# Performance work log

Hardware: AMD Instinct MI355X
Metric: run time of the kernel (lower is better)

## Reference

```python
import jax, jax.numpy as jnp
import numpy as np

NEG_BIG = -9e15
ALPHA = 0.2  # leaky relu slope


def setup_inputs() -> dict:
    key = jax.random.key(0)
    k1, k2, k3, k4 = jax.random.split(key, 4)
    B, N, Fin, Fout = 8, 2048, 128, 64
    h = jax.random.normal(k1, (B, N, Fin), dtype=jnp.float32)
    adj = jax.random.randint(k2, (B, N, N), 0, 2, dtype=jnp.int32)
    # xavier_uniform-like init scale
    W = jax.random.uniform(k3, (Fin, Fout), dtype=jnp.float32, minval=-1.0, maxval=1.0) * (1.414 * np.sqrt(6.0 / (Fin + Fout)))
    a = jax.random.uniform(k4, (2 * Fout, 1), dtype=jnp.float32, minval=-1.0, maxval=1.0) * (1.414 * np.sqrt(6.0 / (2 * Fout + 1)))
    return {"h": h, "adj": adj, "W": W, "a": a}


def reference(h, adj, W, a):
    # h: [B,N,Fin], adj: [B,N,N], W: [Fin,Fout], a: [2*Fout,1]
    Fout = W.shape[1]
    Wh = jnp.einsum('bni,io->bno', h, W)            # [B,N,Fout]
    # e_ij = leakyrelu(a[:Fout] . Wh_i + a[Fout:] . Wh_j)  (decomposed, same math
    # as the original concat + matmul with a)
    f_src = Wh @ a[:Fout, 0]                        # [B,N]
    f_dst = Wh @ a[Fout:, 0]                        # [B,N]
    e = f_src[:, :, None] + f_dst[:, None, :]       # [B,N,N]
    e = jnp.where(e > 0, e, ALPHA * e)              # leaky relu
    e = jnp.where(adj > 0, e, NEG_BIG)              # mask
    attention = jax.nn.softmax(e, axis=2)           # [B,N,N]
    h_prime = jnp.einsum('bnm,bmo->bno', attention, Wh)
    return jax.nn.elu(h_prime)
```

## Files before the change

kernel.cpp:

```cpp
#include <hip/hip_runtime.h>
#include <hip/hip_bf16.h>

constexpr int Bb  = 8;
constexpr int Nn  = 2048;
constexpr int FIN = 128;
constexpr int FOUT = 64;
constexpr float LOG2E = 1.4426950408889634f;

typedef __bf16 bf16x8 __attribute__((ext_vector_type(8)));
typedef __bf16 bf16x2 __attribute__((ext_vector_type(2)));
typedef float  f32x4  __attribute__((ext_vector_type(4)));
typedef int    i32x4  __attribute__((ext_vector_type(4)));
typedef unsigned int u32;

__device__ __forceinline__ u32 f2bf_bits(float f) {
    u32 u = __builtin_bit_cast(u32, f);
    return (u + 0x7FFFu + ((u >> 16) & 1u)) >> 16;
}

__global__ __launch_bounds__(256) void gat_k1(
        const float* __restrict__ h, const float* __restrict__ W,
        const float* __restrict__ a, __bf16* __restrict__ whfrag,
        float* __restrict__ fs, float* __restrict__ fd) {
    const int blk = blockIdx.x;
    const int b   = blk >> 6;
    const int t32 = blk & 63;
    const int n0  = t32 * 32;
    const int l   = threadIdx.x & 63;
    const int w   = __builtin_amdgcn_readfirstlane((int)(threadIdx.x >> 6));

    __shared__ __align__(16) float hT[32][FIN];

    {
        const float4* hb = reinterpret_cast<const float4*>(h + (size_t)(b * Nn + n0) * FIN);
        float4* dst = reinterpret_cast<float4*>(&hT[0][0]);
#pragma unroll
        for (int k = 0; k < 4; ++k) {
            const int flat = threadIdx.x + k * 256;
            dst[flat] = hb[flat];
        }
    }
    __syncthreads();

    const float a0 = a[l];
    const float a1 = a[FOUT + l];

    float acc[8];
#pragma unroll
    for (int r = 0; r < 8; ++r) acc[r] = 0.f;

#pragma unroll 1
    for (int c0 = 0; c0 < FIN; c0 += 32) {
        float wreg[32];
#pragma unroll
        for (int cc = 0; cc < 32; ++cc) wreg[cc] = W[(c0 + cc) * FOUT + l];
#pragma unroll
        for (int r = 0; r < 8; ++r) {
            const int row = w * 8 + r;
#pragma unroll
            for (int cc = 0; cc < 32; ++cc)
                acc[r] = fmaf(hT[row][c0 + cc], wreg[cc], acc[r]);
        }
    }

#pragma unroll
    for (int r = 0; r < 8; ++r) {
        float s0 = acc[r] * a0;
        float s1 = acc[r] * a1;
#pragma unroll
        for (int off = 32; off >= 1; off >>= 1) {
            s0 += __shfl_xor(s0, off, 64);
            s1 += __shfl_xor(s1, off, 64);
        }
        if (l == 0) {
            fs[b * Nn + n0 + w * 8 + r] = s0 * LOG2E;
            fd[b * Nn + n0 + w * 8 + r] = s1 * LOG2E;
        }
    }

    u32 pk[4];
#pragma unroll
    for (int i = 0; i < 4; ++i)
        pk[i] = f2bf_bits(acc[2 * i]) | (f2bf_bits(acc[2 * i + 1]) << 16);
    const int slotg = ((b * 64 + t32) * 4 + (l >> 4)) * 64 + ((w << 4) | (l & 15));
    reinterpret_cast<uint4*>(whfrag)[slotg] = make_uint4(pk[0], pk[1], pk[2], pk[3]);
}

__global__ __launch_bounds__(256, 4) void gat_k2(
        const int* __restrict__ adj, const __bf16* __restrict__ whfrag,
        const float* __restrict__ fs, const float* __restrict__ fd,
        float* __restrict__ out) {
    const int blk = blockIdx.x;
    const int b   = blk >> 7;
    const int i0  = (blk & 127) * 16;
    const int l   = threadIdx.x & 63;
    const int w   = __builtin_amdgcn_readfirstlane((int)(threadIdx.x >> 6));

    __shared__ __align__(16) char  aLDS[4 * 4096];
    __shared__ f32x4 comb[4][4][64];
    __shared__ float zpart[4][16];

    const int g  = l >> 4;
    const int jc = l & 15;

    char* myA = aLDS + w * 4096;

    float fs_loc[4];
#pragma unroll
    for (int rr = 0; rr < 4; ++rr) fs_loc[rr] = fs[b * Nn + i0 + g * 4 + rr];

    const int    jq0  = w * 512;
    const float* fdp  = fd + b * Nn + jq0 + jc * 4;
    const int*   adj0 = adj + (size_t)(b * Nn + i0 + g * 4) * Nn + jq0 + jc * 4;

    const bf16x8* bfr = reinterpret_cast<const bf16x8*>(whfrag)
                        + (size_t)((b * 64 + w * 16) * 4) * 64 + l;

    f32x4 acc[4] = {{0,0,0,0},{0,0,0,0},{0,0,0,0},{0,0,0,0}};
    f32x4 accz   = {0.f, 0.f, 0.f, 0.f};

    bf16x8 onesv;
#pragma unroll
    for (int i = 0; i < 8; ++i) onesv[i] = (__bf16)1.0f;

    i32x4 adjR[3][4];
    f32x4 fdR[3];

#pragma unroll
    for (int rr = 0; rr < 4; ++rr) {
        adjR[0][rr] = *reinterpret_cast<const i32x4*>(adj0 + (size_t)rr * Nn);
        adjR[1][rr] = *reinterpret_cast<const i32x4*>(adj0 + (size_t)rr * Nn + 64);
    }
    fdR[0] = *reinterpret_cast<const f32x4*>(fdp);
    fdR[1] = *reinterpret_cast<const f32x4*>(fdp + 64);

#define GAT_STEP(IT, CUR, PRE)                                                 \
  {                                                                            \
    if ((IT) + 2 < 8) {                \
      _Pragma("unroll")                                                        \
      for (int rr = 0; rr < 4; ++rr)                                           \
        adjR[PRE][rr] = *reinterpret_cast<const i32x4*>(                       \
            adj0 + (size_t)rr * Nn + ((IT) + 2) * 64);                         \
      fdR[PRE] = *reinterpret_cast<const f32x4*>(fdp + ((IT) + 2) * 64);       \
    }                                                                          \
    char* buf = myA + ((IT) & 1) * 2048;                                       \
    _Pragma("unroll")                                                          \
    for (int rr = 0; rr < 4; ++rr) {                                           \
      const int row = g * 4 + rr;                                              \
      u32 wds[2];                                                              \
      _Pragma("unroll")                                                        \
      for (int hp = 0; hp < 2; ++hp) {                                         \
        float pv[2];                                                           \
        _Pragma("unroll")                                                      \
        for (int q = 0; q < 2; ++q) {                                          \
          const int jj = hp * 2 + q;                                           \
          float e  = fs_loc[rr] + fdR[CUR][jj];                                \
          float lr = fmaxf(e, 0.2f * e);          \
          float p  = exp2f(lr);                 \
          pv[q] = (adjR[CUR][rr][jj] > 0) ? p : 0.f;                           \
        }                                                                      \
        wds[hp] = __builtin_bit_cast(u32,                                      \
                      (bf16x2){(__bf16)pv[0], (__bf16)pv[1]});                 \
      }                                                                        \
      const int boff = (row * 128 + jc * 8) ^ ((row & 7) << 4);                \
      *reinterpret_cast<uint2*>(buf + boff) = make_uint2(wds[0], wds[1]);      \
    }                                                                          \
    asm volatile("s_waitcnt lgkmcnt(0)" ::: "memory");                         \
    __builtin_amdgcn_sched_barrier(0x20);            \
    {                                                                          \
      const int rb0 = (((l & 15) * 128 + g * 16) ^ ((l & 7) << 4));            \
      bf16x8 av = *reinterpret_cast<const bf16x8*>(buf + rb0);                 \
      _Pragma("unroll")                                                        \
      for (int o16 = 0; o16 < 4; ++o16)                                        \
        acc[o16] = __builtin_amdgcn_mfma_f32_16x16x32_bf16(                    \
            av, bfr[(((IT) * 2 + 0) * 4 + o16) * 64], acc[o16], 0, 0, 0);      \
      accz = __builtin_amdgcn_mfma_f32_16x16x32_bf16(av, onesv, accz, 0, 0, 0);\
    }                                                                          \
    {                                                                          \
      const int rb1 = (((l & 15) * 128 + 64 + g * 16) ^ ((l & 7) << 4));       \
      bf16x8 av = *reinterpret_cast<const bf16x8*>(buf + rb1);                 \
      _Pragma("unroll")                                                        \
      for (int o16 = 0; o16 < 4; ++o16)                                        \
        acc[o16] = __builtin_amdgcn_mfma_f32_16x16x32_bf16(                    \
            av, bfr[(((IT) * 2 + 1) * 4 + o16) * 64], acc[o16], 0, 0, 0);      \
      accz = __builtin_amdgcn_mfma_f32_16x16x32_bf16(av, onesv, accz, 0, 0, 0);\
    }                                                                          \
  }

    GAT_STEP(0, 0, 2)
    GAT_STEP(1, 1, 0)
    GAT_STEP(2, 2, 1)
    GAT_STEP(3, 0, 2)
    GAT_STEP(4, 1, 0)
    GAT_STEP(5, 2, 1)
    GAT_STEP(6, 0, 2)
    GAT_STEP(7, 1, 0)
#undef GAT_STEP

    if ((l & 15) == 0) {
#pragma unroll
        for (int r = 0; r < 4; ++r) zpart[w][(l >> 4) * 4 + r] = accz[r];
    }
#pragma unroll
    for (int o16 = 0; o16 < 4; ++o16) comb[w][o16][l] = acc[o16];
    __syncthreads();

    f32x4 res = comb[0][w][l];
#pragma unroll
    for (int wp = 1; wp < 4; ++wp) res += comb[wp][w][l];

#pragma unroll
    for (int r = 0; r < 4; ++r) {
        const int row = g * 4 + r;
        float z = zpart[0][row] + zpart[1][row] + zpart[2][row] + zpart[3][row];
        float v = res[r] / z;
        v = v > 0.f ? v : expm1f(v);
        out[(size_t)(b * Nn + i0 + row) * FOUT + w * 16 + jc] = v;
    }
}

extern "C" void kernel_launch(void* const* d_in, const int* in_sizes, int n_in,
                              void* d_out, int out_size, void* d_ws, size_t ws_size,
                              hipStream_t stream) {
    const float* h   = (const float*)d_in[0];
    const int*   adj = (const int*)d_in[1];
    const float* W   = (const float*)d_in[2];
    const float* a   = (const float*)d_in[3];
    float* out = (float*)d_out;

    __bf16* whfrag = (__bf16*)d_ws;
    float*  fs     = (float*)((char*)d_ws + (size_t)Bb * Nn * FOUT * 2);
    float*  fd     = fs + Bb * Nn;

    gat_k1<<<dim3(Bb * 64), dim3(256), 0, stream>>>(h, W, a, whfrag, fs, fd);
    gat_k2<<<dim3(Bb * 128), dim3(256), 0, stream>>>(adj, whfrag, fs, fd, out);
}
```

Baseline: 47.58 us.

## Pre-pack adjacency into bitmasks in a fused pre-kernel and consume bits in the attention kernel

```diff
diff --git a/kernel.cpp b/kernel.cpp
--- a/kernel.cpp
+++ b/kernel.cpp
@@ -10,26 +10,48 @@
 typedef __bf16 bf16x8 __attribute__((ext_vector_type(8)));
 typedef __bf16 bf16x2 __attribute__((ext_vector_type(2)));
 typedef float  f32x4  __attribute__((ext_vector_type(4)));
-typedef int    i32x4  __attribute__((ext_vector_type(4)));
 typedef unsigned int u32;
+typedef unsigned long long u64;
 
 __device__ __forceinline__ u32 f2bf_bits(float f) {
     u32 u = __builtin_bit_cast(u32, f);
     return (u + 0x7FFFu + ((u >> 16) & 1u)) >> 16;
 }
 
-__global__ __launch_bounds__(256) void gat_k1(
-        const float* __restrict__ h, const float* __restrict__ W,
-        const float* __restrict__ a, __bf16* __restrict__ whfrag,
-        float* __restrict__ fs, float* __restrict__ fd) {
+__global__ __launch_bounds__(256) void gat_k01(
+        const float* __restrict__ h, const int* __restrict__ adj,
+        const float* __restrict__ W, const float* __restrict__ a,
+        __bf16* __restrict__ whfrag, float* __restrict__ fs,
+        float* __restrict__ fd, u64* __restrict__ mask) {
+    __shared__ __align__(16) float hT[32][FIN];
+
+    const int l = threadIdx.x & 63;
+    const int w = __builtin_amdgcn_readfirstlane((int)(threadIdx.x >> 6));
+
+    if (blockIdx.x >= 512) {
+        const size_t gw = (size_t)(blockIdx.x - 512) * 4 + w;
+        const int* p   = adj + gw * 4096 + l;
+        u64* mout      = mask + gw * 64;
+#pragma unroll 1
+        for (int i = 0; i < 64; i += 8) {
+            int v[8];
+#pragma unroll
+            for (int k = 0; k < 8; ++k) v[k] = p[(i + k) * 64];
+            u64 m[8];
+#pragma unroll
+            for (int k = 0; k < 8; ++k) m[k] = __ballot(v[k] > 0);
+            if (l == 0) {
+#pragma unroll
+                for (int k = 0; k < 8; ++k) mout[i + k] = m[k];
+            }
+        }
+        return;
+    }
+
     const int blk = blockIdx.x;
     const int b   = blk >> 6;
     const int t32 = blk & 63;
     const int n0  = t32 * 32;
-    const int l   = threadIdx.x & 63;
-    const int w   = __builtin_amdgcn_readfirstlane((int)(threadIdx.x >> 6));
-
-    __shared__ __align__(16) float hT[32][FIN];
 
     {
         const float4* hb = reinterpret_cast<const float4*>(h + (size_t)(b * Nn + n0) * FIN);
@@ -87,7 +109,7 @@
 }
 
 __global__ __launch_bounds__(256, 4) void gat_k2(
-        const int* __restrict__ adj, const __bf16* __restrict__ whfrag,
+        const u64* __restrict__ mask, const __bf16* __restrict__ whfrag,
         const float* __restrict__ fs, const float* __restrict__ fd,
         float* __restrict__ out) {
     const int blk = blockIdx.x;
@@ -102,6 +124,7 @@
 
     const int g  = l >> 4;
     const int jc = l & 15;
+    const int shl = jc * 4;
 
     char* myA = aLDS + w * 4096;
 
@@ -111,7 +134,7 @@
 
     const int    jq0  = w * 512;
     const float* fdp  = fd + b * Nn + jq0 + jc * 4;
-    const int*   adj0 = adj + (size_t)(b * Nn + i0 + g * 4) * Nn + jq0 + jc * 4;
+    const u64*   mkp  = mask + (size_t)(b * Nn + i0 + g * 4) * 32 + w * 8;
 
     const bf16x8* bfr = reinterpret_cast<const bf16x8*>(whfrag)
                         + (size_t)((b * 64 + w * 16) * 4) * 64 + l;
@@ -123,13 +146,13 @@
 #pragma unroll
     for (int i = 0; i < 8; ++i) onesv[i] = (__bf16)1.0f;
 
-    i32x4 adjR[3][4];
+    u64   maskR[3][4];
     f32x4 fdR[3];
 
 #pragma unroll
     for (int rr = 0; rr < 4; ++rr) {
-        adjR[0][rr] = *reinterpret_cast<const i32x4*>(adj0 + (size_t)rr * Nn);
-        adjR[1][rr] = *reinterpret_cast<const i32x4*>(adj0 + (size_t)rr * Nn + 64);
+        maskR[0][rr] = mkp[rr * 32 + 0];
+        maskR[1][rr] = mkp[rr * 32 + 1];
     }
     fdR[0] = *reinterpret_cast<const f32x4*>(fdp);
     fdR[1] = *reinterpret_cast<const f32x4*>(fdp + 64);
@@ -139,14 +162,14 @@
     if ((IT) + 2 < 8) {                \
       _Pragma("unroll")                                                        \
       for (int rr = 0; rr < 4; ++rr)                                           \
-        adjR[PRE][rr] = *reinterpret_cast<const i32x4*>(                       \
-            adj0 + (size_t)rr * Nn + ((IT) + 2) * 64);                         \
+        maskR[PRE][rr] = mkp[rr * 32 + (IT) + 2];                              \
       fdR[PRE] = *reinterpret_cast<const f32x4*>(fdp + ((IT) + 2) * 64);       \
     }                                                                          \
     char* buf = myA + ((IT) & 1) * 2048;                                       \
     _Pragma("unroll")                                                          \
     for (int rr = 0; rr < 4; ++rr) {                                           \
       const int row = g * 4 + rr;                                              \
+      const u32 mm = (u32)(maskR[CUR][rr] >> shl);  \
       u32 wds[2];                                                              \
       _Pragma("unroll")                                                        \
       for (int hp = 0; hp < 2; ++hp) {                                         \
@@ -157,7 +180,7 @@
           float e  = fs_loc[rr] + fdR[CUR][jj];                                \
           float lr = fmaxf(e, 0.2f * e);          \
           float p  = exp2f(lr);                 \
-          pv[q] = (adjR[CUR][rr][jj] > 0) ? p : 0.f;                           \
+          pv[q] = ((mm >> jj) & 1u) ? p : 0.f;                                 \
         }                                                                      \
         wds[hp] = __builtin_bit_cast(u32,                                      \
                       (bf16x2){(__bf16)pv[0], (__bf16)pv[1]});                 \
@@ -231,7 +254,8 @@
     __bf16* whfrag = (__bf16*)d_ws;
     float*  fs     = (float*)((char*)d_ws + (size_t)Bb * Nn * FOUT * 2);
     float*  fd     = fs + Bb * Nn;
-
-    gat_k1<<<dim3(Bb * 64), dim3(256), 0, stream>>>(h, W, a, whfrag, fs, fd);
-    gat_k2<<<dim3(Bb * 128), dim3(256), 0, stream>>>(adj, whfrag, fs, fd, out);
-}
+    u64*    mask   = (u64*)((char*)d_ws + (4u << 20));
+
+    gat_k01<<<dim3(512 + 2048), dim3(256), 0, stream>>>(h, adj, W, a, whfrag, fs, fd, mask);
+    gat_k2 <<<dim3(Bb * 128),   dim3(256), 0, stream>>>(mask, whfrag, fs, fd, out);
+}
```

New measurement: 52.08 us. 9.4% more time.

## Fuse projection and attention kernels via cooperative launch with grid sync

Applied to the files above, without the earlier changes.

```diff
diff --git a/kernel.cpp b/kernel.cpp
--- a/kernel.cpp
+++ b/kernel.cpp
@@ -1,5 +1,8 @@
 #include <hip/hip_runtime.h>
 #include <hip/hip_bf16.h>
+#include <hip/hip_cooperative_groups.h>
+
+namespace cg = cooperative_groups;
 
 constexpr int Bb  = 8;
 constexpr int Nn  = 2048;
@@ -18,36 +21,25 @@
     return (u + 0x7FFFu + ((u >> 16) & 1u)) >> 16;
 }
 
-__global__ __launch_bounds__(256) void gat_k1(
+__device__ __forceinline__ void k1_body(
         const float* __restrict__ h, const float* __restrict__ W,
         const float* __restrict__ a, __bf16* __restrict__ whfrag,
-        float* __restrict__ fs, float* __restrict__ fd) {
-    const int blk = blockIdx.x;
-    const int b   = blk >> 6;
-    const int t32 = blk & 63;
-    const int n0  = t32 * 32;
-    const int l   = threadIdx.x & 63;
-    const int w   = __builtin_amdgcn_readfirstlane((int)(threadIdx.x >> 6));
-
-    __shared__ __align__(16) float hT[32][FIN];
-
+        float* __restrict__ fsg, float* __restrict__ fd, float* fs_lds,
+        float (*hT)[FIN], int b, int i0, int l, int w, int tid) {
     {
-        const float4* hb = reinterpret_cast<const float4*>(h + (size_t)(b * Nn + n0) * FIN);
+        const float4* hb = reinterpret_cast<const float4*>(h + (size_t)(b * Nn + i0) * FIN);
         float4* dst = reinterpret_cast<float4*>(&hT[0][0]);
-#pragma unroll
-        for (int k = 0; k < 4; ++k) {
-            const int flat = threadIdx.x + k * 256;
-            dst[flat] = hb[flat];
-        }
+        dst[tid]       = hb[tid];
+        dst[tid + 256] = hb[tid + 256];
     }
     __syncthreads();
 
     const float a0 = a[l];
     const float a1 = a[FOUT + l];
 
-    float acc[8];
-#pragma unroll
-    for (int r = 0; r < 8; ++r) acc[r] = 0.f;
+    float acc[4];
+#pragma unroll
+    for (int r = 0; r < 4; ++r) acc[r] = 0.f;
 
 #pragma unroll 1
     for (int c0 = 0; c0 < FIN; c0 += 32) {
@@ -55,8 +47,8 @@
 #pragma unroll
         for (int cc = 0; cc < 32; ++cc) wreg[cc] = W[(c0 + cc) * FOUT + l];
 #pragma unroll
-        for (int r = 0; r < 8; ++r) {
-            const int row = w * 8 + r;
+        for (int r = 0; r < 4; ++r) {
+            const int row = w * 4 + r;
 #pragma unroll
             for (int cc = 0; cc < 32; ++cc)
                 acc[r] = fmaf(hT[row][c0 + cc], wreg[cc], acc[r]);
@@ -64,7 +56,7 @@
     }
 
 #pragma unroll
-    for (int r = 0; r < 8; ++r) {
+    for (int r = 0; r < 4; ++r) {
         float s0 = acc[r] * a0;
         float s1 = acc[r] * a1;
 #pragma unroll
@@ -73,49 +65,28 @@
             s1 += __shfl_xor(s1, off, 64);
         }
         if (l == 0) {
-            fs[b * Nn + n0 + w * 8 + r] = s0 * LOG2E;
-            fd[b * Nn + n0 + w * 8 + r] = s1 * LOG2E;
+            fs_lds[w * 4 + r] = s0 * LOG2E;
+            fsg[b * Nn + i0 + w * 4 + r] = s0 * LOG2E;
+            fd [b * Nn + i0 + w * 4 + r] = s1 * LOG2E;
         }
     }
 
-    u32 pk[4];
-#pragma unroll
-    for (int i = 0; i < 4; ++i)
-        pk[i] = f2bf_bits(acc[2 * i]) | (f2bf_bits(acc[2 * i + 1]) << 16);
-    const int slotg = ((b * 64 + t32) * 4 + (l >> 4)) * 64 + ((w << 4) | (l & 15));
-    reinterpret_cast<uint4*>(whfrag)[slotg] = make_uint4(pk[0], pk[1], pk[2], pk[3]);
-}
-
-__global__ __launch_bounds__(256, 4) void gat_k2(
-        const int* __restrict__ adj, const __bf16* __restrict__ whfrag,
-        const float* __restrict__ fs, const float* __restrict__ fd,
-        float* __restrict__ out) {
-    const int blk = blockIdx.x;
-    const int b   = blk >> 7;
-    const int i0  = (blk & 127) * 16;
-    const int l   = threadIdx.x & 63;
-    const int w   = __builtin_amdgcn_readfirstlane((int)(threadIdx.x >> 6));
-
-    __shared__ __align__(16) char  aLDS[4 * 4096];
-    __shared__ f32x4 comb[4][4][64];
-    __shared__ float zpart[4][16];
-
-    const int g  = l >> 4;
-    const int jc = l & 15;
-
-    char* myA = aLDS + w * 4096;
-
-    float fs_loc[4];
-#pragma unroll
-    for (int rr = 0; rr < 4; ++rr) fs_loc[rr] = fs[b * Nn + i0 + g * 4 + rr];
-
-    const int    jq0  = w * 512;
-    const float* fdp  = fd + b * Nn + jq0 + jc * 4;
-    const int*   adj0 = adj + (size_t)(b * Nn + i0 + g * 4) * Nn + jq0 + jc * 4;
-
-    const bf16x8* bfr = reinterpret_cast<const bf16x8*>(whfrag)
-                        + (size_t)((b * 64 + w * 16) * 4) * 64 + l;
-
+    const u32 pk0 = f2bf_bits(acc[0]) | (f2bf_bits(acc[1]) << 16);
+    const u32 pk1 = f2bf_bits(acc[2]) | (f2bf_bits(acc[3]) << 16);
+    const int t32  = i0 >> 5;
+    const int half = (i0 >> 4) & 1;
+    const int Lc   = ((half * 2 + (w >> 1)) << 4) | (l & 15);
+    const int slot = ((b * 64 + t32) * 4 + (l >> 4)) * 64 + Lc;
+    *reinterpret_cast<uint2*>(reinterpret_cast<char*>(whfrag)
+                              + (size_t)slot * 16 + (w & 1) * 8) = make_uint2(pk0, pk1);
+}
+
+__device__ __forceinline__ void k2_body(
+        const int* __restrict__ adj0, const float* __restrict__ fdp,
+        const bf16x8* __restrict__ bfr, const float fs_loc[4],
+        char* myA, f32x4 (*comb)[4][64], float (*zpart)[16],
+        float* __restrict__ out, int b, int i0, int l, int w, int g, int jc,
+        i32x4 (&adjR)[3][4]) {
     f32x4 acc[4] = {{0,0,0,0},{0,0,0,0},{0,0,0,0},{0,0,0,0}};
     f32x4 accz   = {0.f, 0.f, 0.f, 0.f};
 
@@ -123,20 +94,13 @@
 #pragma unroll
     for (int i = 0; i < 8; ++i) onesv[i] = (__bf16)1.0f;
 
-    i32x4 adjR[3][4];
     f32x4 fdR[3];
-
-#pragma unroll
-    for (int rr = 0; rr < 4; ++rr) {
-        adjR[0][rr] = *reinterpret_cast<const i32x4*>(adj0 + (size_t)rr * Nn);
-        adjR[1][rr] = *reinterpret_cast<const i32x4*>(adj0 + (size_t)rr * Nn + 64);
-    }
     fdR[0] = *reinterpret_cast<const f32x4*>(fdp);
     fdR[1] = *reinterpret_cast<const f32x4*>(fdp + 64);
 
 #define GAT_STEP(IT, CUR, PRE)                                                 \
   {                                                                            \
-    if ((IT) + 2 < 8) {                \
+    if ((IT) + 2 < 8) {                                                        \
       _Pragma("unroll")                                                        \
       for (int rr = 0; rr < 4; ++rr)                                           \
         adjR[PRE][rr] = *reinterpret_cast<const i32x4*>(                       \
@@ -219,6 +183,95 @@
     }
 }
 
+__global__ __launch_bounds__(256, 4) void gat_fused(
+        const float* __restrict__ h, const int* __restrict__ adj,
+        const float* __restrict__ W, const float* __restrict__ a,
+        __bf16* __restrict__ whfrag, float* __restrict__ fsg,
+        float* __restrict__ fd, float* __restrict__ out) {
+    __shared__ __align__(16) char  aLDS[4 * 4096];
+    __shared__ __align__(16) f32x4 comb[4][4][64];
+    __shared__ float zpart[4][16];
+    __shared__ float fs_lds[16];
+
+    const int blk = blockIdx.x;
+    const int b   = blk & 7;
+    const int i0  = (blk >> 3) * 16;
+    const int l   = threadIdx.x & 63;
+    const int w   = __builtin_amdgcn_readfirstlane((int)(threadIdx.x >> 6));
+
+    float (*hT)[FIN] = reinterpret_cast<float(*)[FIN]>(&comb[0][0][0]);
+    k1_body(h, W, a, whfrag, fsg, fd, fs_lds, hT, b, i0, l, w, (int)threadIdx.x);
+
+    const int g = l >> 4, jc = l & 15;
+    const int* adj0 = adj + (size_t)(b * Nn + i0 + g * 4) * Nn + w * 512 + jc * 4;
+    i32x4 adjR[3][4];
+#pragma unroll
+    for (int rr = 0; rr < 4; ++rr) {
+        adjR[0][rr] = *reinterpret_cast<const i32x4*>(adj0 + (size_t)rr * Nn);
+        adjR[1][rr] = *reinterpret_cast<const i32x4*>(adj0 + (size_t)rr * Nn + 64);
+    }
+
+    cg::this_grid().sync();
+
+    float fs_loc[4];
+#pragma unroll
+    for (int rr = 0; rr < 4; ++rr) fs_loc[rr] = fs_lds[g * 4 + rr];
+    const float* fdp = fd + b * Nn + w * 512 + jc * 4;
+    const bf16x8* bfr = reinterpret_cast<const bf16x8*>(whfrag)
+                        + (size_t)((b * 64 + w * 16) * 4) * 64 + l;
+
+    k2_body(adj0, fdp, bfr, fs_loc, aLDS + w * 4096, comb, zpart, out,
+            b, i0, l, w, g, jc, adjR);
+}
+
+__global__ __launch_bounds__(256) void gat_k1_fast(
+        const float* __restrict__ h, const float* __restrict__ W,
+        const float* __restrict__ a, __bf16* __restrict__ whfrag,
+        float* __restrict__ fsg, float* __restrict__ fd) {
+    __shared__ __align__(16) float hT[16][FIN];
+    __shared__ float fs_lds[16];
+    const int blk = blockIdx.x;
+    const int b   = blk & 7;
+    const int i0  = (blk >> 3) * 16;
+    const int l   = threadIdx.x & 63;
+    const int w   = __builtin_amdgcn_readfirstlane((int)(threadIdx.x >> 6));
+    k1_body(h, W, a, whfrag, fsg, fd, fs_lds, hT, b, i0, l, w, (int)threadIdx.x);
+}
+
+__global__ __launch_bounds__(256, 4) void gat_k2(
+        const int* __restrict__ adj, const __bf16* __restrict__ whfrag,
+        const float* __restrict__ fsg, const float* __restrict__ fd,
+        float* __restrict__ out) {
+    __shared__ __align__(16) char  aLDS[4 * 4096];
+    __shared__ __align__(16) f32x4 comb[4][4][64];
+    __shared__ float zpart[4][16];
+
+    const int blk = blockIdx.x;
+    const int b   = blk & 7;
+    const int i0  = (blk >> 3) * 16;
+    const int l   = threadIdx.x & 63;
+    const int w   = __builtin_amdgcn_readfirstlane((int)(threadIdx.x >> 6));
+
+    const int g = l >> 4, jc = l & 15;
+    const int* adj0 = adj + (size_t)(b * Nn + i0 + g * 4) * Nn + w * 512 + jc * 4;
+    i32x4 adjR[3][4];
+#pragma unroll
+    for (int rr = 0; rr < 4; ++rr) {
+        adjR[0][rr] = *reinterpret_cast<const i32x4*>(adj0 + (size_t)rr * Nn);
+        adjR[1][rr] = *reinterpret_cast<const i32x4*>(adj0 + (size_t)rr * Nn + 64);
+    }
+
+    float fs_loc[4];
+#pragma unroll
+    for (int rr = 0; rr < 4; ++rr) fs_loc[rr] = fsg[b * Nn + i0 + g * 4 + rr];
+    const float* fdp = fd + b * Nn + w * 512 + jc * 4;
+    const bf16x8* bfr = reinterpret_cast<const bf16x8*>(whfrag)
+                        + (size_t)((b * 64 + w * 16) * 4) * 64 + l;
+
+    k2_body(adj0, fdp, bfr, fs_loc, aLDS + w * 4096, comb, zpart, out,
+            b, i0, l, w, g, jc, adjR);
+}
+
 extern "C" void kernel_launch(void* const* d_in, const int* in_sizes, int n_in,
                               void* d_out, int out_size, void* d_ws, size_t ws_size,
                               hipStream_t stream) {
@@ -229,9 +282,15 @@
     float* out = (float*)d_out;
 
     __bf16* whfrag = (__bf16*)d_ws;
-    float*  fs     = (float*)((char*)d_ws + (size_t)Bb * Nn * FOUT * 2);
-    float*  fd     = fs + Bb * Nn;
-
-    gat_k1<<<dim3(Bb * 64), dim3(256), 0, stream>>>(h, W, a, whfrag, fs, fd);
-    gat_k2<<<dim3(Bb * 128), dim3(256), 0, stream>>>(adj, whfrag, fs, fd, out);
-}
+    float*  fsg    = (float*)((char*)d_ws + (size_t)Bb * Nn * FOUT * 2);
+    float*  fd     = fsg + Bb * Nn;
+
+    void* kargs[] = { (void*)&h, (void*)&adj, (void*)&W, (void*)&a,
+                      (void*)&whfrag, (void*)&fsg, (void*)&fd, (void*)&out };
+    hipError_t e = hipLaunchCooperativeKernel(
+        reinterpret_cast<void*>(gat_fused), dim3(1024), dim3(256), kargs, 0, stream);
+    if (e != hipSuccess) {
+        gat_k1_fast<<<dim3(1024), dim3(256), 0, stream>>>(h, W, a, whfrag, fsg, fd);
+        gat_k2    <<<dim3(1024), dim3(256), 0, stream>>>(adj, whfrag, fsg, fd, out);
+    }
+}
```

Result: slower. 177.4 us (+272.8%).
